# Optimization experiments

Hardware: AMD Instinct MI355X
Metric: run time of the kernel (lower is better)

## Reference

```python
import jax, jax.numpy as jnp
import numpy as np

E, H, I = 8, 2048, 768  # num_experts, hidden_size, moe_intermediate_size
B, S = 4, 1024


def setup_inputs() -> dict:
    key = jax.random.key(0)
    k1, k2, k3, k4, k5 = jax.random.split(key, 5)
    hidden_states = jax.random.normal(k1, (B, S, H), dtype=jnp.float32)
    routing_weights = jax.random.uniform(k2, (B * S, E), dtype=jnp.float32)
    router_indices = jax.random.randint(k3, (B * S, 2), 0, E)
    gate_up_proj = jax.random.normal(k4, (E, H, 2 * I), dtype=jnp.float32) * 0.02
    down_proj = jax.random.normal(k5, (E, I, H), dtype=jnp.float32) * 0.02
    return {
        "hidden_states": hidden_states,
        "routing_weights": routing_weights,
        "router_indices": router_indices,
        "gate_up_proj": gate_up_proj,
        "down_proj": down_proj,
    }


def reference(hidden_states, routing_weights, router_indices, gate_up_proj, down_proj):
    b, s, h = hidden_states.shape
    x = hidden_states.reshape(-1, h)  # [T, H], T = B*S
    # dense all-experts: every token through every expert
    gate_up = jnp.einsum("th,ehd->etd", x, gate_up_proj)  # [E, T, 2I]
    gate, up = jnp.split(gate_up, 2, axis=-1)
    inter = up * jax.nn.silu(gate)  # [E, T, I]
    out = jnp.einsum("eti,eih->eth", inter, down_proj)  # [E, T, H]
    rw = routing_weights.T.reshape(out.shape[0], b, s)  # [E, B, S]
    out = out.reshape(out.shape[0], b, s, h) * rw[..., None]
    return out.sum(axis=0)  # [B, S, H]
```

## Files before the change

kernel.cpp:

```cpp
#include <hip/hip_runtime.h>
#include <cstdint>
#include <cstddef>

#define NE 8
#define NH 2048
#define NI 768
#define NT 4096
#define NK2 6144

typedef __bf16 bf16x8 __attribute__((ext_vector_type(8)));
typedef float f32x4 __attribute__((ext_vector_type(4)));
typedef unsigned short u16x8 __attribute__((ext_vector_type(8)));

__device__ __forceinline__ unsigned short f2bf(float f) {
  unsigned int u = __builtin_bit_cast(unsigned int, f);
  u += 0x7fffu + ((u >> 16) & 1u);
  return (unsigned short)(u >> 16);
}

__device__ __forceinline__ void gload_lds16(const void* g, void* s) {
  __builtin_amdgcn_global_load_lds(
      (const __attribute__((address_space(1))) unsigned int*)g,
      (__attribute__((address_space(3))) unsigned int*)s, 16, 0, 0);
}

__global__ __launch_bounds__(256) void k_cvt(const float* __restrict__ in,
                                             unsigned short* __restrict__ out,
                                             long n) {
  long i = ((long)blockIdx.x * blockDim.x + threadIdx.x) * 8;
  if (i >= n) return;
  float4 f0 = *reinterpret_cast<const float4*>(in + i);
  float4 f1 = *reinterpret_cast<const float4*>(in + i + 4);
  u16x8 o;
  o[0] = f2bf(f0.x); o[1] = f2bf(f0.y); o[2] = f2bf(f0.z); o[3] = f2bf(f0.w);
  o[4] = f2bf(f1.x); o[5] = f2bf(f1.y); o[6] = f2bf(f1.z); o[7] = f2bf(f1.w);
  *reinterpret_cast<u16x8*>(out + i) = o;
}

__global__ __launch_bounds__(256) void k_transpose_cvt(
    const float* __restrict__ in, unsigned short* __restrict__ out,
    int R, int C, long inBS, long outBS, int outCS, int mode) {
  __shared__ float tile[32][33];
  const int b = blockIdx.z;
  const int r0 = blockIdx.y * 32, c0 = blockIdx.x * 32;
  const int tx = threadIdx.x, ty = threadIdx.y;
  const float* ib = in + (long)b * inBS;
#pragma unroll
  for (int d = 0; d < 4; d++)
    tile[ty + d * 8][tx] = ib[(long)(r0 + ty + d * 8) * C + c0 + tx];
  __syncthreads();
#pragma unroll
  for (int d = 0; d < 4; d++) {
    int c = c0 + ty + d * 8;
    int r = r0 + tx;
    int orow;
    if (mode == 1) {
      int z = (c >= NI) ? 1 : 0;
      int cc = c - z * NI;
      orow = ((cc >> 4) << 5) + (z << 4) + (cc & 15);
    } else {
      orow = c;
    }
    out[(long)b * outBS + (long)orow * outCS + r] = f2bf(tile[tx][ty + d * 8]);
  }
}


#define BUF_US 24576
#define B_OFF 16384

__device__ __forceinline__ void gemm_core(
    const unsigned short* __restrict__ A, int ldA, int rowA0,
    const unsigned short* __restrict__ B, int ldB, int rowB0,
    int nkt, unsigned short* lds, f32x4 acc[4][4]) {
  const int tid = threadIdx.x;
  const int lane = tid & 63;
  const int wave = tid >> 6;
  const int wr = wave >> 1;
  const int wc = wave & 1;
  const int fr = lane & 15, fq = lane >> 4;

  size_t sA[4]; int dA[4];
#pragma unroll
  for (int q = 0; q < 4; ++q) {
    int chunk = q * 512 + tid;
    int row = chunk >> 3, c = chunk & 7;
    sA[q] = (size_t)(rowA0 + row) * ldA + ((c ^ (row & 7)) << 3);
    dA[q] = chunk * 8;
  }
  size_t sB[2]; int dB[2];
#pragma unroll
  for (int q = 0; q < 2; ++q) {
    int chunk = q * 512 + tid;
    int row = chunk >> 3, c = chunk & 7;
    sB[q] = (size_t)(rowB0 + row) * ldB + ((c ^ (row & 7)) << 3);
    dB[q] = B_OFF + chunk * 8;
  }

  int aO[2][4], bO[2][4];
#pragma unroll
  for (int kk = 0; kk < 2; ++kk) {
#pragma unroll
    for (int i = 0; i < 4; ++i) {
      int rowA = wr * 64 + i * 16 + fr;
      aO[kk][i] = rowA * 64 + (((kk * 4 + fq) ^ (rowA & 7)) << 3);
      int rowB = wc * 64 + i * 16 + fr;
      bO[kk][i] = B_OFF + rowB * 64 + (((kk * 4 + fq) ^ (rowB & 7)) << 3);
    }
  }

#pragma unroll
  for (int i = 0; i < 4; ++i)
#pragma unroll
    for (int j = 0; j < 4; ++j) acc[i][j] = (f32x4){0.f, 0.f, 0.f, 0.f};

#pragma unroll
  for (int q = 0; q < 4; ++q) gload_lds16(A + sA[q], lds + dA[q]);
#pragma unroll
  for (int q = 0; q < 2; ++q) gload_lds16(B + sB[q], lds + dB[q]);
#pragma unroll
  for (int q = 0; q < 4; ++q) gload_lds16(A + sA[q] + 64, lds + BUF_US + dA[q]);
#pragma unroll
  for (int q = 0; q < 2; ++q) gload_lds16(B + sB[q] + 64, lds + BUF_US + dB[q]);

  int bi = 0;
  int bs = 2;
  for (int kt = 0; kt < nkt; ++kt) {
    if (kt == nkt - 1) {
      asm volatile("s_waitcnt vmcnt(0)" ::: "memory");
    } else {
      asm volatile("s_waitcnt vmcnt(6)" ::: "memory");
    }
    __builtin_amdgcn_s_barrier();
    __builtin_amdgcn_sched_barrier(0);

    if (kt + 2 < nkt) {
      const int k0 = (kt + 2) * 64;
      unsigned short* tb = lds + bs * BUF_US;
#pragma unroll
      for (int q = 0; q < 4; ++q) gload_lds16(A + sA[q] + k0, tb + dA[q]);
#pragma unroll
      for (int q = 0; q < 2; ++q) gload_lds16(B + sB[q] + k0, tb + dB[q]);
    }

    const unsigned short* cb = lds + bi * BUF_US;
#pragma unroll
    for (int kk = 0; kk < 2; ++kk) {
      bf16x8 a[4], b[4];
#pragma unroll
      for (int i = 0; i < 4; ++i) a[i] = *reinterpret_cast<const bf16x8*>(cb + aO[kk][i]);
#pragma unroll
      for (int j = 0; j < 4; ++j) b[j] = *reinterpret_cast<const bf16x8*>(cb + bO[kk][j]);
      __builtin_amdgcn_s_setprio(1);
#pragma unroll
      for (int i = 0; i < 4; ++i)
#pragma unroll
        for (int j = 0; j < 4; ++j)
          acc[i][j] = __builtin_amdgcn_mfma_f32_16x16x32_bf16(a[i], b[j], acc[i][j], 0, 0, 0);
      __builtin_amdgcn_s_setprio(0);
    }

    bi = (bi == 2) ? 0 : bi + 1;
    bs = (bs == 2) ? 0 : bs + 1;
  }
}

__global__ __launch_bounds__(512, 2) void k_gemm1(
    const unsigned short* __restrict__ Xb,
    const unsigned short* __restrict__ W1t,
    const float* __restrict__ rw,
    unsigned short* __restrict__ inter) {
  __shared__ unsigned short lds[3 * BUF_US];
  const int e = blockIdx.z;
  const int t0 = blockIdx.y * 256;
  const int bn = blockIdx.x;
  f32x4 acc[4][4];
  gemm_core(Xb, NH, t0, W1t + (size_t)e * (2 * NI) * NH, NH, bn * 128,
            NH / 64, lds, acc);

  const int tid = threadIdx.x, lane = tid & 63, wave = tid >> 6;
  const int wr = wave >> 1, wc = wave & 1, fr = lane & 15, fq = lane >> 4;
  const int rowBase = t0 + wr * 64 + fq * 4;
#pragma unroll
  for (int i = 0; i < 4; ++i) {
#pragma unroll
    for (int r = 0; r < 4; ++r) {
      const int t = rowBase + i * 16 + r;
      const float rwv = rw[(size_t)t * NE + e];
#pragma unroll
      for (int p = 0; p < 2; ++p) {
        float g = acc[i][2 * p][r];
        float u = acc[i][2 * p + 1][r];
        float s = g / (1.f + __expf(-g));
        int col = bn * 64 + wc * 32 + p * 16 + fr;
        inter[(size_t)t * NK2 + e * NI + col] = f2bf(rwv * u * s);
      }
    }
  }
}

__global__ __launch_bounds__(512, 2) void k_gemm2(
    const unsigned short* __restrict__ inter,
    const unsigned short* __restrict__ W2t,
    float* __restrict__ out) {
  __shared__ unsigned short lds[3 * BUF_US];
  const int t0 = blockIdx.y * 256;
  const int h0 = blockIdx.x * 128;
  f32x4 acc[4][4];
  gemm_core(inter, NK2, t0, W2t, NK2, h0, NK2 / 64, lds, acc);

  const int tid = threadIdx.x, lane = tid & 63, wave = tid >> 6;
  const int wr = wave >> 1, wc = wave & 1, fr = lane & 15, fq = lane >> 4;
  const int rowBase = t0 + wr * 64 + fq * 4;
#pragma unroll
  for (int i = 0; i < 4; ++i)
#pragma unroll
    for (int j = 0; j < 4; ++j)
#pragma unroll
      for (int r = 0; r < 4; ++r)
        out[(size_t)(rowBase + i * 16 + r) * NH + h0 + wc * 64 + j * 16 + fr] =
            acc[i][j][r];
}

extern "C" void kernel_launch(void* const* d_in, const int* in_sizes, int n_in,
                              void* d_out, int out_size, void* d_ws, size_t ws_size,
                              hipStream_t stream) {
  const float* x = (const float*)d_in[0];
  const float* rw = (const float*)d_in[1];
  const float* w1 = (const float*)d_in[3];
  const float* w2 = (const float*)d_in[4];
  float* out = (float*)d_out;

  char* ws = (char*)d_ws;
  unsigned short* Xb = (unsigned short*)ws;
  unsigned short* W1t = (unsigned short*)(ws + 16777216);
  unsigned short* W2t = (unsigned short*)(ws + 16777216 + 50331648);
  unsigned short* inter = (unsigned short*)(ws + 16777216 + 50331648 + 25165824);

  k_cvt<<<dim3((NT * NH) / (256 * 8)), dim3(256), 0, stream>>>(x, Xb, (long)NT * NH);
  k_transpose_cvt<<<dim3((2 * NI) / 32, NH / 32, NE), dim3(32, 8), 0, stream>>>(
      w1, W1t, NH, 2 * NI, (long)NH * 2 * NI, (long)2 * NI * NH, NH, 1);
  k_transpose_cvt<<<dim3(NH / 32, NI / 32, NE), dim3(32, 8), 0, stream>>>(
      w2, W2t, NI, NH, (long)NI * NH, (long)NI, NK2, 0);
  k_gemm1<<<dim3((2 * NI) / 128, NT / 256, NE), dim3(512), 0, stream>>>(Xb, W1t, rw, inter);
  k_gemm2<<<dim3(NH / 128, NT / 256), dim3(512), 0, stream>>>(inter, W2t, out);
}
```

Before: 378.0 us.

## Rewrite gemm1 with 256x256 tiles and an eight-phase interleaved LDS pipeline

The first expert GEMM now uses its own kernel with a 256x256 output tile instead of 256x128, which halves the number of N-blocks and raises operand reuse per LDS load. The K loop is split into eight quarter-tile phases per two K-steps, each issuing a slice of the next global-to-LDS loads between barriers with double buffering, so memory traffic overlaps MFMA work. In exchange each wave holds twice the accumulators (8x4 fragments), which raises register pressure at the 512x2 launch bound, and the kernel has more barriers. It also launches fewer blocks.

```diff
diff --git a/kernel.cpp b/kernel.cpp
--- a/kernel.cpp
+++ b/kernel.cpp
@@ -66,6 +66,141 @@
 }
 
 
+__global__ __launch_bounds__(512, 2) void k_gemm1(
+    const unsigned short* __restrict__ Xb,
+    const unsigned short* __restrict__ W1t,
+    const float* __restrict__ rw,
+    unsigned short* __restrict__ inter) {
+  __shared__ unsigned short lds[2][2][16384];
+
+  const int e = blockIdx.z;
+  const int t0 = blockIdx.y * 256;
+  const int bn = blockIdx.x;
+  const int tid = threadIdx.x;
+  const int lane = tid & 63;
+  const int wave = tid >> 6;
+  const int wr = wave >> 2, wc = wave & 3;
+  const int fr = lane & 15, fq = lane >> 4;
+
+  const unsigned short* Ag = Xb;
+  const unsigned short* Bg = W1t + (size_t)e * (2 * NI) * NH;
+  const int rowA0 = t0, rowB0 = bn * 256;
+  const int nkt = NH / 64;
+  const int NIT = nkt / 2;
+
+  const int cl0 = tid, cl1 = 512 + tid;
+  const int rih0 = cl0 >> 3, ck0 = cl0 & 7;
+  const int rih1 = cl1 >> 3, ck1 = cl1 & 7;
+  const unsigned short* sA0q0 = Ag + (size_t)(rowA0 + rih0) * NH + ((ck0 ^ (rih0 & 7)) << 3);
+  const unsigned short* sA0q1 = Ag + (size_t)(rowA0 + rih1) * NH + ((ck1 ^ (rih1 & 7)) << 3);
+  const unsigned short* sA1q0 = Ag + (size_t)(rowA0 + 128 + rih0) * NH + ((ck0 ^ (rih0 & 7)) << 3);
+  const unsigned short* sA1q1 = Ag + (size_t)(rowA0 + 128 + rih1) * NH + ((ck1 ^ (rih1 & 7)) << 3);
+  const unsigned short* sB0q0 = Bg + (size_t)(rowB0 + rih0) * NH + ((ck0 ^ (rih0 & 7)) << 3);
+  const unsigned short* sB0q1 = Bg + (size_t)(rowB0 + rih1) * NH + ((ck1 ^ (rih1 & 7)) << 3);
+  const unsigned short* sB1q0 = Bg + (size_t)(rowB0 + 128 + rih0) * NH + ((ck0 ^ (rih0 & 7)) << 3);
+  const unsigned short* sB1q1 = Bg + (size_t)(rowB0 + 128 + rih1) * NH + ((ck1 ^ (rih1 & 7)) << 3);
+  const int d0 = cl0 * 8, d1 = cl1 * 8;
+
+#define STG_A(BUFI, H, KT) do { \
+    gload_lds16(sA##H##q0 + (size_t)(KT) * 64, &lds[BUFI][0][(H) * 8192 + d0]); \
+    gload_lds16(sA##H##q1 + (size_t)(KT) * 64, &lds[BUFI][0][(H) * 8192 + d1]); \
+  } while (0)
+#define STG_B(BUFI, H, KT) do { \
+    gload_lds16(sB##H##q0 + (size_t)(KT) * 64, &lds[BUFI][1][(H) * 8192 + d0]); \
+    gload_lds16(sB##H##q1 + (size_t)(KT) * 64, &lds[BUFI][1][(H) * 8192 + d1]); \
+  } while (0)
+
+  f32x4 acc[8][4];
+#pragma unroll
+  for (int i = 0; i < 8; ++i)
+#pragma unroll
+    for (int j = 0; j < 4; ++j) acc[i][j] = (f32x4){0.f, 0.f, 0.f, 0.f};
+
+  const int swz = fr & 7;
+
+#define PHASE(BUFI, IH, JH, ISSUE, DOWAIT) do { \
+    bf16x8 af[4][2], bf[2][2]; \
+    _Pragma("unroll") \
+    for (int ii = 0; ii < 4; ++ii) { \
+      const int rA = (IH) * 128 + wr * 64 + ii * 16 + fr; \
+      _Pragma("unroll") \
+      for (int kk = 0; kk < 2; ++kk) \
+        af[ii][kk] = *reinterpret_cast<const bf16x8*>( \
+            &lds[BUFI][0][rA * 64 + (((kk * 4 + fq) ^ swz) << 3)]); \
+    } \
+    _Pragma("unroll") \
+    for (int jj = 0; jj < 2; ++jj) { \
+      const int rB = (JH) * 128 + wc * 32 + jj * 16 + fr; \
+      _Pragma("unroll") \
+      for (int kk = 0; kk < 2; ++kk) \
+        bf[jj][kk] = *reinterpret_cast<const bf16x8*>( \
+            &lds[BUFI][1][rB * 64 + (((kk * 4 + fq) ^ swz) << 3)]); \
+    } \
+    ISSUE; \
+    if (DOWAIT) asm volatile("s_waitcnt vmcnt(4)" ::: "memory"); \
+    __builtin_amdgcn_sched_barrier(0); \
+    __builtin_amdgcn_s_barrier(); \
+    __builtin_amdgcn_sched_barrier(0); \
+    __builtin_amdgcn_s_setprio(1); \
+    _Pragma("unroll") \
+    for (int kk = 0; kk < 2; ++kk) \
+      _Pragma("unroll") \
+      for (int ii = 0; ii < 4; ++ii) \
+        _Pragma("unroll") \
+        for (int jj = 0; jj < 2; ++jj) \
+          acc[(IH) * 4 + ii][(JH) * 2 + jj] = __builtin_amdgcn_mfma_f32_16x16x32_bf16( \
+              af[ii][kk], bf[jj][kk], acc[(IH) * 4 + ii][(JH) * 2 + jj], 0, 0, 0); \
+    __builtin_amdgcn_s_setprio(0); \
+    __builtin_amdgcn_sched_barrier(0); \
+    __builtin_amdgcn_s_barrier(); \
+    __builtin_amdgcn_sched_barrier(0); \
+  } while (0)
+
+  STG_B(0, 0, 0); STG_A(0, 0, 0); STG_A(0, 1, 0); STG_B(0, 1, 0);
+  STG_B(1, 0, 1); STG_A(1, 0, 1);
+  asm volatile("s_waitcnt vmcnt(4)" ::: "memory");
+  __builtin_amdgcn_sched_barrier(0);
+  __builtin_amdgcn_s_barrier();
+  __builtin_amdgcn_sched_barrier(0);
+
+  for (int it = 0; it < NIT; ++it) {
+    const int kt1 = 2 * it + 1;
+    const int p0 = (2 * it + 2 < nkt) ? 2 * it + 2 : nkt - 1;
+    const int p1 = (2 * it + 3 < nkt) ? 2 * it + 3 : nkt - 1;
+    PHASE(0, 0, 0, STG_A(1, 1, kt1), 0);
+    PHASE(0, 1, 0, STG_B(1, 1, kt1), 0);
+    PHASE(0, 0, 1, STG_B(0, 0, p0), 0);
+    PHASE(0, 1, 1, STG_A(0, 0, p0), 1);
+    PHASE(1, 0, 0, STG_A(0, 1, p0), 0);
+    PHASE(1, 1, 0, STG_B(0, 1, p0), 0);
+    PHASE(1, 0, 1, STG_B(1, 0, p1), 0);
+    PHASE(1, 1, 1, STG_A(1, 0, p1), 1);
+  }
+  asm volatile("s_waitcnt vmcnt(0)" ::: "memory");
+
+#undef PHASE
+#undef STG_A
+#undef STG_B
+
+#pragma unroll
+  for (int i = 0; i < 8; ++i) {
+    const int trow = t0 + (i >> 2) * 128 + wr * 64 + (i & 3) * 16 + fq * 4;
+#pragma unroll
+    for (int r = 0; r < 4; ++r) {
+      const int t = trow + r;
+      const float rwv = rw[(size_t)t * NE + e];
+#pragma unroll
+      for (int p = 0; p < 2; ++p) {
+        float g = acc[i][2 * p][r];
+        float u = acc[i][2 * p + 1][r];
+        float s = g / (1.f + __expf(-g));
+        const int col = bn * 128 + (p * 4 + wc) * 16 + fr;
+        inter[(size_t)t * NK2 + e * NI + col] = f2bf(rwv * u * s);
+      }
+    }
+  }
+}
+
 #define BUF_US 24576
 #define B_OFF 16384
 
@@ -123,8 +258,7 @@
 #pragma unroll
   for (int q = 0; q < 2; ++q) gload_lds16(B + sB[q] + 64, lds + BUF_US + dB[q]);
 
-  int bi = 0;
-  int bs = 2;
+  int bi = 0, bs = 2;
   for (int kt = 0; kt < nkt; ++kt) {
     if (kt == nkt - 1) {
       asm volatile("s_waitcnt vmcnt(0)" ::: "memory");
@@ -162,40 +296,6 @@
 
     bi = (bi == 2) ? 0 : bi + 1;
     bs = (bs == 2) ? 0 : bs + 1;
-  }
-}
-
-__global__ __launch_bounds__(512, 2) void k_gemm1(
-    const unsigned short* __restrict__ Xb,
-    const unsigned short* __restrict__ W1t,
-    const float* __restrict__ rw,
-    unsigned short* __restrict__ inter) {
-  __shared__ unsigned short lds[3 * BUF_US];
-  const int e = blockIdx.z;
-  const int t0 = blockIdx.y * 256;
-  const int bn = blockIdx.x;
-  f32x4 acc[4][4];
-  gemm_core(Xb, NH, t0, W1t + (size_t)e * (2 * NI) * NH, NH, bn * 128,
-            NH / 64, lds, acc);
-
-  const int tid = threadIdx.x, lane = tid & 63, wave = tid >> 6;
-  const int wr = wave >> 1, wc = wave & 1, fr = lane & 15, fq = lane >> 4;
-  const int rowBase = t0 + wr * 64 + fq * 4;
-#pragma unroll
-  for (int i = 0; i < 4; ++i) {
-#pragma unroll
-    for (int r = 0; r < 4; ++r) {
-      const int t = rowBase + i * 16 + r;
-      const float rwv = rw[(size_t)t * NE + e];
-#pragma unroll
-      for (int p = 0; p < 2; ++p) {
-        float g = acc[i][2 * p][r];
-        float u = acc[i][2 * p + 1][r];
-        float s = g / (1.f + __expf(-g));
-        int col = bn * 64 + wc * 32 + p * 16 + fr;
-        inter[(size_t)t * NK2 + e * NI + col] = f2bf(rwv * u * s);
-      }
-    }
   }
 }
 
@@ -242,6 +342,6 @@
       w1, W1t, NH, 2 * NI, (long)NH * 2 * NI, (long)2 * NI * NH, NH, 1);
   k_transpose_cvt<<<dim3(NH / 32, NI / 32, NE), dim3(32, 8), 0, stream>>>(
       w2, W2t, NI, NH, (long)NI * NH, (long)NI, NK2, 0);
-  k_gemm1<<<dim3((2 * NI) / 128, NT / 256, NE), dim3(512), 0, stream>>>(Xb, W1t, rw, inter);
+  k_gemm1<<<dim3((2 * NI) / 256, NT / 256, NE), dim3(512), 0, stream>>>(Xb, W1t, rw, inter);
   k_gemm2<<<dim3(NH / 128, NT / 256), dim3(512), 0, stream>>>(inter, W2t, out);
 }
```

Result: no change. 372.2 us (-1.5%).

## Enlarge gemm1 tile to 256x256 and switch both GEMMs to double-buffered pipelines

Applied to the files above, without the earlier changes.

gemm1 now computes a 256x256 output tile per block, with 8x4 MFMA fragments per wave in a 2x4 wave grid, which halves the grid and raises arithmetic intensity per staged byte. Both GEMMs drop the shared triple-buffered core for an inlined double-buffered loop that issues the next stage's loads at the top of each iteration and adds a second barrier per k-step. The larger accumulator set raises register pressure and may lower occupancy. The redundant reload of the last stage on the final iteration also adds some waste.

```diff
diff --git a/kernel.cpp b/kernel.cpp
--- a/kernel.cpp
+++ b/kernel.cpp
@@ -66,133 +66,120 @@
 }
 
 
-#define BUF_US 24576
-#define B_OFF 16384
-
-__device__ __forceinline__ void gemm_core(
-    const unsigned short* __restrict__ A, int ldA, int rowA0,
-    const unsigned short* __restrict__ B, int ldB, int rowB0,
-    int nkt, unsigned short* lds, f32x4 acc[4][4]) {
-  const int tid = threadIdx.x;
-  const int lane = tid & 63;
-  const int wave = tid >> 6;
-  const int wr = wave >> 1;
-  const int wc = wave & 1;
-  const int fr = lane & 15, fq = lane >> 4;
-
-  size_t sA[4]; int dA[4];
-#pragma unroll
-  for (int q = 0; q < 4; ++q) {
-    int chunk = q * 512 + tid;
-    int row = chunk >> 3, c = chunk & 7;
-    sA[q] = (size_t)(rowA0 + row) * ldA + ((c ^ (row & 7)) << 3);
-    dA[q] = chunk * 8;
-  }
-  size_t sB[2]; int dB[2];
-#pragma unroll
-  for (int q = 0; q < 2; ++q) {
-    int chunk = q * 512 + tid;
-    int row = chunk >> 3, c = chunk & 7;
-    sB[q] = (size_t)(rowB0 + row) * ldB + ((c ^ (row & 7)) << 3);
-    dB[q] = B_OFF + chunk * 8;
-  }
-
-  int aO[2][4], bO[2][4];
-#pragma unroll
-  for (int kk = 0; kk < 2; ++kk) {
-#pragma unroll
-    for (int i = 0; i < 4; ++i) {
-      int rowA = wr * 64 + i * 16 + fr;
-      aO[kk][i] = rowA * 64 + (((kk * 4 + fq) ^ (rowA & 7)) << 3);
-      int rowB = wc * 64 + i * 16 + fr;
-      bO[kk][i] = B_OFF + rowB * 64 + (((kk * 4 + fq) ^ (rowB & 7)) << 3);
-    }
-  }
-
-#pragma unroll
-  for (int i = 0; i < 4; ++i)
-#pragma unroll
-    for (int j = 0; j < 4; ++j) acc[i][j] = (f32x4){0.f, 0.f, 0.f, 0.f};
-
-#pragma unroll
-  for (int q = 0; q < 4; ++q) gload_lds16(A + sA[q], lds + dA[q]);
-#pragma unroll
-  for (int q = 0; q < 2; ++q) gload_lds16(B + sB[q], lds + dB[q]);
-#pragma unroll
-  for (int q = 0; q < 4; ++q) gload_lds16(A + sA[q] + 64, lds + BUF_US + dA[q]);
-#pragma unroll
-  for (int q = 0; q < 2; ++q) gload_lds16(B + sB[q] + 64, lds + BUF_US + dB[q]);
-
-  int bi = 0;
-  int bs = 2;
-  for (int kt = 0; kt < nkt; ++kt) {
-    if (kt == nkt - 1) {
-      asm volatile("s_waitcnt vmcnt(0)" ::: "memory");
-    } else {
-      asm volatile("s_waitcnt vmcnt(6)" ::: "memory");
-    }
-    __builtin_amdgcn_s_barrier();
-    __builtin_amdgcn_sched_barrier(0);
-
-    if (kt + 2 < nkt) {
-      const int k0 = (kt + 2) * 64;
-      unsigned short* tb = lds + bs * BUF_US;
-#pragma unroll
-      for (int q = 0; q < 4; ++q) gload_lds16(A + sA[q] + k0, tb + dA[q]);
-#pragma unroll
-      for (int q = 0; q < 2; ++q) gload_lds16(B + sB[q] + k0, tb + dB[q]);
-    }
-
-    const unsigned short* cb = lds + bi * BUF_US;
-#pragma unroll
-    for (int kk = 0; kk < 2; ++kk) {
-      bf16x8 a[4], b[4];
-#pragma unroll
-      for (int i = 0; i < 4; ++i) a[i] = *reinterpret_cast<const bf16x8*>(cb + aO[kk][i]);
-#pragma unroll
-      for (int j = 0; j < 4; ++j) b[j] = *reinterpret_cast<const bf16x8*>(cb + bO[kk][j]);
-      __builtin_amdgcn_s_setprio(1);
-#pragma unroll
-      for (int i = 0; i < 4; ++i)
-#pragma unroll
-        for (int j = 0; j < 4; ++j)
-          acc[i][j] = __builtin_amdgcn_mfma_f32_16x16x32_bf16(a[i], b[j], acc[i][j], 0, 0, 0);
-      __builtin_amdgcn_s_setprio(0);
-    }
-
-    bi = (bi == 2) ? 0 : bi + 1;
-    bs = (bs == 2) ? 0 : bs + 1;
-  }
-}
-
 __global__ __launch_bounds__(512, 2) void k_gemm1(
     const unsigned short* __restrict__ Xb,
     const unsigned short* __restrict__ W1t,
     const float* __restrict__ rw,
     unsigned short* __restrict__ inter) {
-  __shared__ unsigned short lds[3 * BUF_US];
+  __shared__ unsigned short ldsA[2][16384];
+  __shared__ unsigned short ldsB[2][16384];
+
   const int e = blockIdx.z;
   const int t0 = blockIdx.y * 256;
   const int bn = blockIdx.x;
-  f32x4 acc[4][4];
-  gemm_core(Xb, NH, t0, W1t + (size_t)e * (2 * NI) * NH, NH, bn * 128,
-            NH / 64, lds, acc);
-
-  const int tid = threadIdx.x, lane = tid & 63, wave = tid >> 6;
-  const int wr = wave >> 1, wc = wave & 1, fr = lane & 15, fq = lane >> 4;
-  const int rowBase = t0 + wr * 64 + fq * 4;
-#pragma unroll
-  for (int i = 0; i < 4; ++i) {
+  const int tid = threadIdx.x;
+  const int lane = tid & 63, wave = tid >> 6;
+  const int wr = wave >> 2, wc = wave & 3;
+  const int fr = lane & 15, fq = lane >> 4;
+  const int nkt = NH / 64;
+
+  const unsigned short* Bg = W1t + (size_t)e * (2 * NI) * NH;
+  const int rih = tid >> 3, ck = tid & 7;
+  const unsigned short* sA = Xb + (size_t)(t0 + rih) * NH + ((ck ^ (rih & 7)) << 3);
+  const unsigned short* sB = Bg + (size_t)(bn * 256 + rih) * NH + ((ck ^ (rih & 7)) << 3);
+  const int dst = tid * 8;
+
+#define STG1(C) do { \
+    const int cc_ = (C); \
+    unsigned short* da_ = &ldsA[cc_ & 1][dst]; \
+    unsigned short* db_ = &ldsB[cc_ & 1][dst]; \
+    const size_t ko_ = (size_t)cc_ * 64; \
+    _Pragma("unroll") \
+    for (int q = 0; q < 4; ++q) { \
+      gload_lds16(sA + ko_ + (size_t)q * (64 * NH), da_ + q * 4096); \
+      gload_lds16(sB + ko_ + (size_t)q * (64 * NH), db_ + q * 4096); \
+    } \
+  } while (0)
+
+  f32x4 acc[8][4];
+#pragma unroll
+  for (int i = 0; i < 8; ++i)
+#pragma unroll
+    for (int j = 0; j < 4; ++j) acc[i][j] = (f32x4){0.f, 0.f, 0.f, 0.f};
+
+  const int swz = fr & 7;
+  int aoff[8], boff[4];
+#pragma unroll
+  for (int i = 0; i < 8; ++i)
+    aoff[i] = ((i >> 2) * 128 + wr * 64 + (i & 3) * 16 + fr) * 64 + ((fq ^ swz) << 3);
+#pragma unroll
+  for (int j = 0; j < 4; ++j)
+    boff[j] = ((j >> 1) * 128 + wc * 32 + (j & 1) * 16 + fr) * 64 + ((fq ^ swz) << 3);
+  const int dk = ((((4 + fq) ^ swz) - (fq ^ swz)) << 3);
+
+  STG1(0);
+  STG1(1);
+
+  for (int kt = 0; kt < nkt; ++kt) {
+    const int cur = kt & 1;
+    const int nx = (kt + 1 < nkt) ? kt + 1 : nkt - 1;
+    STG1(nx);
+    asm volatile("s_waitcnt vmcnt(8)" ::: "memory");
+    __builtin_amdgcn_sched_barrier(0);
+    __builtin_amdgcn_s_barrier();
+    __builtin_amdgcn_sched_barrier(0);
+    {
+      bf16x8 af[8], bf[4];
+#pragma unroll
+      for (int i = 0; i < 8; ++i)
+        af[i] = *reinterpret_cast<const bf16x8*>(&ldsA[cur][aoff[i]]);
+#pragma unroll
+      for (int j = 0; j < 4; ++j)
+        bf[j] = *reinterpret_cast<const bf16x8*>(&ldsB[cur][boff[j]]);
+      __builtin_amdgcn_s_setprio(1);
+#pragma unroll
+      for (int i = 0; i < 8; ++i)
+#pragma unroll
+        for (int j = 0; j < 4; ++j)
+          acc[i][j] = __builtin_amdgcn_mfma_f32_16x16x32_bf16(af[i], bf[j], acc[i][j], 0, 0, 0);
+      __builtin_amdgcn_s_setprio(0);
+    }
+    {
+      bf16x8 af[8], bf[4];
+#pragma unroll
+      for (int i = 0; i < 8; ++i)
+        af[i] = *reinterpret_cast<const bf16x8*>(&ldsA[cur][aoff[i] + dk]);
+#pragma unroll
+      for (int j = 0; j < 4; ++j)
+        bf[j] = *reinterpret_cast<const bf16x8*>(&ldsB[cur][boff[j] + dk]);
+      __builtin_amdgcn_sched_barrier(0);
+      __builtin_amdgcn_s_barrier();
+      __builtin_amdgcn_sched_barrier(0);
+      __builtin_amdgcn_s_setprio(1);
+#pragma unroll
+      for (int i = 0; i < 8; ++i)
+#pragma unroll
+        for (int j = 0; j < 4; ++j)
+          acc[i][j] = __builtin_amdgcn_mfma_f32_16x16x32_bf16(af[i], bf[j], acc[i][j], 0, 0, 0);
+      __builtin_amdgcn_s_setprio(0);
+    }
+  }
+  asm volatile("s_waitcnt vmcnt(0)" ::: "memory");
+#undef STG1
+
+#pragma unroll
+  for (int i = 0; i < 8; ++i) {
+    const int trow = t0 + (i >> 2) * 128 + wr * 64 + (i & 3) * 16 + fq * 4;
 #pragma unroll
     for (int r = 0; r < 4; ++r) {
-      const int t = rowBase + i * 16 + r;
+      const int t = trow + r;
       const float rwv = rw[(size_t)t * NE + e];
 #pragma unroll
       for (int p = 0; p < 2; ++p) {
         float g = acc[i][2 * p][r];
         float u = acc[i][2 * p + 1][r];
         float s = g / (1.f + __expf(-g));
-        int col = bn * 64 + wc * 32 + p * 16 + fr;
+        const int col = bn * 128 + (p * 4 + wc) * 16 + fr;
         inter[(size_t)t * NK2 + e * NI + col] = f2bf(rwv * u * s);
       }
     }
@@ -203,14 +190,101 @@
     const unsigned short* __restrict__ inter,
     const unsigned short* __restrict__ W2t,
     float* __restrict__ out) {
-  __shared__ unsigned short lds[3 * BUF_US];
+  __shared__ unsigned short ldsA[2][16384];
+  __shared__ unsigned short ldsB[2][8192];
+
   const int t0 = blockIdx.y * 256;
   const int h0 = blockIdx.x * 128;
+  const int tid = threadIdx.x;
+  const int lane = tid & 63, wave = tid >> 6;
+  const int wr = wave >> 1, wc = wave & 1;
+  const int fr = lane & 15, fq = lane >> 4;
+  const int nkt = NK2 / 64;
+
+  const int rih = tid >> 3, ck = tid & 7;
+  const unsigned short* sA = inter + (size_t)(t0 + rih) * NK2 + ((ck ^ (rih & 7)) << 3);
+  const unsigned short* sB = W2t + (size_t)(h0 + rih) * NK2 + ((ck ^ (rih & 7)) << 3);
+  const int dst = tid * 8;
+
+#define STG2(C) do { \
+    const int cc_ = (C); \
+    unsigned short* da_ = &ldsA[cc_ & 1][dst]; \
+    unsigned short* db_ = &ldsB[cc_ & 1][dst]; \
+    const size_t ko_ = (size_t)cc_ * 64; \
+    _Pragma("unroll") \
+    for (int q = 0; q < 4; ++q) \
+      gload_lds16(sA + ko_ + (size_t)q * (64 * NK2), da_ + q * 4096); \
+    _Pragma("unroll") \
+    for (int q = 0; q < 2; ++q) \
+      gload_lds16(sB + ko_ + (size_t)q * (64 * NK2), db_ + q * 4096); \
+  } while (0)
+
   f32x4 acc[4][4];
-  gemm_core(inter, NK2, t0, W2t, NK2, h0, NK2 / 64, lds, acc);
-
-  const int tid = threadIdx.x, lane = tid & 63, wave = tid >> 6;
-  const int wr = wave >> 1, wc = wave & 1, fr = lane & 15, fq = lane >> 4;
+#pragma unroll
+  for (int i = 0; i < 4; ++i)
+#pragma unroll
+    for (int j = 0; j < 4; ++j) acc[i][j] = (f32x4){0.f, 0.f, 0.f, 0.f};
+
+  const int swz = fr & 7;
+  int aoff[4], boff[4];
+#pragma unroll
+  for (int i = 0; i < 4; ++i)
+    aoff[i] = (wr * 64 + i * 16 + fr) * 64 + ((fq ^ swz) << 3);
+#pragma unroll
+  for (int j = 0; j < 4; ++j)
+    boff[j] = (wc * 64 + j * 16 + fr) * 64 + ((fq ^ swz) << 3);
+  const int dk = ((((4 + fq) ^ swz) - (fq ^ swz)) << 3);
+
+  STG2(0);
+  STG2(1);
+
+  for (int kt = 0; kt < nkt; ++kt) {
+    const int cur = kt & 1;
+    const int nx = (kt + 1 < nkt) ? kt + 1 : nkt - 1;
+    STG2(nx);
+    asm volatile("s_waitcnt vmcnt(6)" ::: "memory");
+    __builtin_amdgcn_sched_barrier(0);
+    __builtin_amdgcn_s_barrier();
+    __builtin_amdgcn_sched_barrier(0);
+    {
+      bf16x8 af[4], bf[4];
+#pragma unroll
+      for (int i = 0; i < 4; ++i)
+        af[i] = *reinterpret_cast<const bf16x8*>(&ldsA[cur][aoff[i]]);
+#pragma unroll
+      for (int j = 0; j < 4; ++j)
+        bf[j] = *reinterpret_cast<const bf16x8*>(&ldsB[cur][boff[j]]);
+      __builtin_amdgcn_s_setprio(1);
+#pragma unroll
+      for (int i = 0; i < 4; ++i)
+#pragma unroll
+        for (int j = 0; j < 4; ++j)
+          acc[i][j] = __builtin_amdgcn_mfma_f32_16x16x32_bf16(af[i], bf[j], acc[i][j], 0, 0, 0);
+      __builtin_amdgcn_s_setprio(0);
+    }
+    {
+      bf16x8 af[4], bf[4];
+#pragma unroll
+      for (int i = 0; i < 4; ++i)
+        af[i] = *reinterpret_cast<const bf16x8*>(&ldsA[cur][aoff[i] + dk]);
+#pragma unroll
+      for (int j = 0; j < 4; ++j)
+        bf[j] = *reinterpret_cast<const bf16x8*>(&ldsB[cur][boff[j] + dk]);
+      __builtin_amdgcn_sched_barrier(0);
+      __builtin_amdgcn_s_barrier();
+      __builtin_amdgcn_sched_barrier(0);
+      __builtin_amdgcn_s_setprio(1);
+#pragma unroll
+      for (int i = 0; i < 4; ++i)
+#pragma unroll
+        for (int j = 0; j < 4; ++j)
+          acc[i][j] = __builtin_amdgcn_mfma_f32_16x16x32_bf16(af[i], bf[j], acc[i][j], 0, 0, 0);
+      __builtin_amdgcn_s_setprio(0);
+    }
+  }
+  asm volatile("s_waitcnt vmcnt(0)" ::: "memory");
+#undef STG2
+
   const int rowBase = t0 + wr * 64 + fq * 4;
 #pragma unroll
   for (int i = 0; i < 4; ++i)
@@ -242,6 +316,6 @@
       w1, W1t, NH, 2 * NI, (long)NH * 2 * NI, (long)2 * NI * NH, NH, 1);
   k_transpose_cvt<<<dim3(NH / 32, NI / 32, NE), dim3(32, 8), 0, stream>>>(
       w2, W2t, NI, NH, (long)NI * NH, (long)NI, NK2, 0);
-  k_gemm1<<<dim3((2 * NI) / 128, NT / 256, NE), dim3(512), 0, stream>>>(Xb, W1t, rw, inter);
+  k_gemm1<<<dim3((2 * NI) / 256, NT / 256, NE), dim3(512), 0, stream>>>(Xb, W1t, rw, inter);
   k_gemm2<<<dim3(NH / 128, NT / 256), dim3(512), 0, stream>>>(inter, W2t, out);
 }
```

After: 366.9 us. 2.9% less time.

## Rewrite gemm1 mainloop with BK=32, 4-stage LDS ring and register double-buffered fragments

Applied to the files above, without the earlier changes.

Replaces the shared gemm_core call in k_gemm1 with a dedicated mainloop that uses 32-wide K tiles in a 4-deep LDS ring, prefetching three stages ahead. LDS fragments for the next tile are read into alternate register sets while MFMAs run on the current set, with one barrier per K-step. It is meant to hide LDS and global latency behind MFMA work. Launch bounds drop to one block per CU, which lowers occupancy, and the tile layout uses a new paired-row swizzle.

```diff
diff --git a/kernel.cpp b/kernel.cpp
--- a/kernel.cpp
+++ b/kernel.cpp
@@ -65,6 +65,122 @@
   }
 }
 
+__global__ __launch_bounds__(512, 1) void k_gemm1(
+    const unsigned short* __restrict__ Xb,
+    const unsigned short* __restrict__ W1t,
+    const float* __restrict__ rw,
+    unsigned short* __restrict__ inter) {
+  __shared__ unsigned short lds[4][12288];
+
+  const int e = blockIdx.z;
+  const int t0 = blockIdx.y * 256;
+  const int bn = blockIdx.x;
+  const int tid = threadIdx.x;
+  const int lane = tid & 63, wave = tid >> 6;
+  const int wr = wave >> 1, wc = wave & 1;
+  const int fr = lane & 15, fq = lane >> 4;
+  const int nkt = NH / 32;
+
+  const unsigned short* Bg = W1t + (size_t)e * (2 * NI) * NH;
+
+  int r0c, k0c, r1c, k1c;
+  {
+    int c = tid, pr = c >> 3, pc = c & 7, pcl = pc ^ (pr & 7);
+    r0c = (pr << 1) | (pcl >> 2); k0c = pcl & 3;
+    c = tid + 512; pr = c >> 3; pc = c & 7; pcl = pc ^ (pr & 7);
+    r1c = (pr << 1) | (pcl >> 2); k1c = pcl & 3;
+  }
+  const unsigned short* sA0 = Xb + (size_t)(t0 + r0c) * NH + k0c * 8;
+  const unsigned short* sA1 = Xb + (size_t)(t0 + r1c) * NH + k1c * 8;
+  const unsigned short* sB0 = Bg + (size_t)(bn * 128 + r0c) * NH + k0c * 8;
+  const int dst0 = tid * 8, dst1 = tid * 8 + 4096;
+
+#define STG1(T) do { \
+    unsigned short* L_ = lds[(T) & 3]; const size_t ko_ = (size_t)(T) * 32; \
+    gload_lds16(sA0 + ko_, L_ + dst0); \
+    gload_lds16(sA1 + ko_, L_ + dst1); \
+    gload_lds16(sB0 + ko_, L_ + 8192 + dst0); \
+  } while (0)
+
+  f32x4 acc[4][4];
+#pragma unroll
+  for (int i = 0; i < 4; ++i)
+#pragma unroll
+    for (int j = 0; j < 4; ++j) acc[i][j] = (f32x4){0.f, 0.f, 0.f, 0.f};
+
+  int aoff[4], boff[4];
+#pragma unroll
+  for (int m = 0; m < 4; ++m) {
+    const int rA = wr * 64 + m * 16 + fr;
+    const int pr = rA >> 1;
+    const int pcs = (((rA & 1) << 2) | fq) ^ (pr & 7);
+    aoff[m] = pr * 64 + pcs * 8;
+  }
+#pragma unroll
+  for (int j = 0; j < 4; ++j) {
+    const int rB = wc * 64 + j * 16 + fr;
+    const int pr = rB >> 1;
+    const int pcs = (((rB & 1) << 2) | fq) ^ (pr & 7);
+    boff[j] = 8192 + pr * 64 + pcs * 8;
+  }
+
+#define READ1(T, F) do { \
+    const unsigned short* L_ = lds[(T) & 3]; \
+    _Pragma("unroll") \
+    for (int m = 0; m < 4; ++m) F[m] = *reinterpret_cast<const bf16x8*>(L_ + aoff[m]); \
+    _Pragma("unroll") \
+    for (int j = 0; j < 4; ++j) F[4 + j] = *reinterpret_cast<const bf16x8*>(L_ + boff[j]); \
+  } while (0)
+
+#define REGION1(KT, CUR, NXT) do { \
+    const int kt_ = (KT); \
+    if (kt_ + 1 < nkt) READ1(kt_ + 1, NXT); \
+    if (kt_ + 3 < nkt) STG1(kt_ + 3); \
+    __builtin_amdgcn_s_setprio(1); \
+    _Pragma("unroll") \
+    for (int m = 0; m < 4; ++m) \
+      _Pragma("unroll") \
+      for (int j = 0; j < 4; ++j) \
+        acc[m][j] = __builtin_amdgcn_mfma_f32_16x16x32_bf16(CUR[m], CUR[4 + j], acc[m][j], 0, 0, 0); \
+    __builtin_amdgcn_s_setprio(0); \
+    if (kt_ + 3 < nkt)      { asm volatile("s_waitcnt vmcnt(3)" ::: "memory"); } \
+    else if (kt_ + 2 < nkt) { asm volatile("s_waitcnt vmcnt(0)" ::: "memory"); } \
+    if (kt_ + 1 < nkt)      { asm volatile("s_barrier" ::: "memory"); } \
+  } while (0)
+
+  STG1(0); STG1(1); STG1(2);
+  asm volatile("s_waitcnt vmcnt(3)" ::: "memory");
+  asm volatile("s_barrier" ::: "memory");
+
+  bf16x8 fE[8], fO[8];
+  READ1(0, fE);
+  for (int i = 0; i < nkt / 2; ++i) {
+    REGION1(2 * i, fE, fO);
+    REGION1(2 * i + 1, fO, fE);
+  }
+  asm volatile("s_waitcnt vmcnt(0)" ::: "memory");
+#undef REGION1
+#undef READ1
+#undef STG1
+
+  const int rowBase = t0 + wr * 64 + fq * 4;
+#pragma unroll
+  for (int i = 0; i < 4; ++i) {
+#pragma unroll
+    for (int r = 0; r < 4; ++r) {
+      const int t = rowBase + i * 16 + r;
+      const float rwv = rw[(size_t)t * NE + e];
+#pragma unroll
+      for (int p = 0; p < 2; ++p) {
+        float g = acc[i][2 * p][r];
+        float u = acc[i][2 * p + 1][r];
+        float s = g / (1.f + __expf(-g));
+        const int col = bn * 64 + (wc * 2 + p) * 16 + fr;
+        inter[(size_t)t * NK2 + e * NI + col] = f2bf(rwv * u * s);
+      }
+    }
+  }
+}
 
 #define BUF_US 24576
 #define B_OFF 16384
@@ -123,8 +239,7 @@
 #pragma unroll
   for (int q = 0; q < 2; ++q) gload_lds16(B + sB[q] + 64, lds + BUF_US + dB[q]);
 
-  int bi = 0;
-  int bs = 2;
+  int bi = 0, bs = 2;
   for (int kt = 0; kt < nkt; ++kt) {
     if (kt == nkt - 1) {
       asm volatile("s_waitcnt vmcnt(0)" ::: "memory");
@@ -162,40 +277,6 @@
 
     bi = (bi == 2) ? 0 : bi + 1;
     bs = (bs == 2) ? 0 : bs + 1;
-  }
-}
-
-__global__ __launch_bounds__(512, 2) void k_gemm1(
-    const unsigned short* __restrict__ Xb,
-    const unsigned short* __restrict__ W1t,
-    const float* __restrict__ rw,
-    unsigned short* __restrict__ inter) {
-  __shared__ unsigned short lds[3 * BUF_US];
-  const int e = blockIdx.z;
-  const int t0 = blockIdx.y * 256;
-  const int bn = blockIdx.x;
-  f32x4 acc[4][4];
-  gemm_core(Xb, NH, t0, W1t + (size_t)e * (2 * NI) * NH, NH, bn * 128,
-            NH / 64, lds, acc);
-
-  const int tid = threadIdx.x, lane = tid & 63, wave = tid >> 6;
-  const int wr = wave >> 1, wc = wave & 1, fr = lane & 15, fq = lane >> 4;
-  const int rowBase = t0 + wr * 64 + fq * 4;
-#pragma unroll
-  for (int i = 0; i < 4; ++i) {
-#pragma unroll
-    for (int r = 0; r < 4; ++r) {
-      const int t = rowBase + i * 16 + r;
-      const float rwv = rw[(size_t)t * NE + e];
-#pragma unroll
-      for (int p = 0; p < 2; ++p) {
-        float g = acc[i][2 * p][r];
-        float u = acc[i][2 * p + 1][r];
-        float s = g / (1.f + __expf(-g));
-        int col = bn * 64 + wc * 32 + p * 16 + fr;
-        inter[(size_t)t * NK2 + e * NI + col] = f2bf(rwv * u * s);
-      }
-    }
   }
 }
 
```

Result: slower. 399.4 us (+5.7%).
